# Kernel optimization log

Measured on AMD Instinct MI355X. Metric: run time of the kernel, lower is better.

Reference implementation:

```python
import jax, jax.numpy as jnp
import numpy as np

B, T, C = 1, 2048, 1024
H = 16
HD = C // H  # 64
K = 8
EPS = 1e-6
NEG = -1.0e9


def apply_rotary_emb(x, cos, sin):
    # x: (B,T,H,HD), cos/sin: (T, HD//2)
    x1, x2 = jnp.split(x, 2, axis=-1)
    c = cos[None, :, None, :]
    s = sin[None, :, None, :]
    return jnp.concatenate([x1 * c - x2 * s, x1 * s + x2 * c], axis=-1)


def rms_norm(x):
    return x * jax.lax.rsqrt(jnp.mean(jnp.square(x), axis=-1, keepdims=True) + EPS)


def setup_inputs() -> dict:
    key = jax.random.key(0)
    ks = jax.random.split(key, 8)
    x = jax.random.normal(ks[0], (B, T, C), dtype=jnp.float32)
    # standard RoPE tables
    inv_freq = 1.0 / (10000.0 ** (np.arange(0, HD, 2, dtype=np.float32) / HD))
    t = np.arange(T, dtype=np.float32)
    freqs = np.outer(t, inv_freq)  # (T, HD//2)
    cos = jnp.asarray(np.cos(freqs), dtype=jnp.float32)
    sin = jnp.asarray(np.sin(freqs), dtype=jnp.float32)
    std = 0.02
    Wq = std * jax.random.normal(ks[1], (C, C), dtype=jnp.float32)
    Wk = std * jax.random.normal(ks[2], (C, C), dtype=jnp.float32)
    Wv = std * jax.random.normal(ks[3], (C, C), dtype=jnp.float32)
    Wproj = std * jax.random.normal(ks[4], (C, C), dtype=jnp.float32)
    Wdq = jax.random.normal(ks[5], (C, K), dtype=jnp.float32) / np.sqrt(C)
    Wdk = jax.random.normal(ks[6], (C, K), dtype=jnp.float32) / np.sqrt(C)
    return {"x": x, "cos": cos, "sin": sin, "Wq": Wq, "Wk": Wk, "Wv": Wv,
            "Wproj": Wproj, "Wdq": Wdq, "Wdk": Wdk}


def reference(x, cos, sin, Wq, Wk, Wv, Wproj, Wdq, Wdk):
    b, t, c = x.shape
    q = (x @ Wq).reshape(b, t, H, HD)
    k = (x @ Wk).reshape(b, t, H, HD)
    v = (x @ Wv).reshape(b, t, H, HD)
    q = rms_norm(apply_rotary_emb(q, cos, sin))
    k = rms_norm(apply_rotary_emb(k, cos, sin))

    # digit projections (identical for every head in the source module)
    qd = x @ Wdq  # (B,T,K)
    kd = x @ Wdk  # (B,T,K)
    matches = qd[:, :, None, :] == kd[:, None, :, :]  # (B,Tq,Tk,K)
    prefix = jnp.cumprod(matches.astype(jnp.int32), axis=-1)
    lcp = jnp.sum(prefix, axis=-1)  # (B,Tq,Tk)
    lcp_mask = lcp >= (K - 1)

    causal = jnp.tril(jnp.ones((t, t), dtype=bool))
    combined = causal[None, None, :, :] & lcp_mask[:, None, :, :]  # (B,1->H,Tq,Tk)

    scale = 1.0 / jnp.sqrt(jnp.asarray(HD, x.dtype))
    scores = jnp.einsum('bqhd,bkhd->bhqk', q * scale, k)
    scores = jnp.where(combined, scores, NEG)
    w = jax.nn.softmax(scores, axis=-1)
    y = jnp.einsum('bhqk,bkhd->bqhd', w, v).reshape(b, t, c)
    return y @ Wproj
```

## Files before the change

kernel.cpp:

```cpp
#include <hip/hip_runtime.h>
#include <math.h>

#define T_DIM 2048
#define C_DIM 1024
#define H_NUM 16
#define HD_DIM 64
#define K_LCP 8
#define NEG_VAL -1.0e9f

typedef __bf16 bf16;
typedef __bf16 bf16x4 __attribute__((ext_vector_type(4)));
typedef __bf16 bf16x8 __attribute__((ext_vector_type(8)));
typedef float f32x4 __attribute__((ext_vector_type(4)));
typedef unsigned long long u64;

__global__ __launch_bounds__(256) void fused_a(
    const float* __restrict__ x, const float* __restrict__ Wdq,
    const float* __restrict__ Wdk, const float* __restrict__ Wq,
    const float* __restrict__ Wk, const float* __restrict__ Wv,
    const float* __restrict__ Wproj, bf16* __restrict__ xb,
    float* __restrict__ qd, float* __restrict__ kd, float* __restrict__ partial,
    int* __restrict__ flags, float* __restrict__ vmean,
    float* __restrict__ rowout, bf16* __restrict__ wqt, bf16* __restrict__ wkt,
    bf16* __restrict__ wvt, bf16* __restrict__ wpt) {
  __shared__ bf16 tile[64][67];
  const int vb = blockIdx.x;
  const int tid = threadIdx.x;
  if (vb < 512) {
    const int wave = tid >> 6, lane = tid & 63;
    const int t = vb * 4 + wave;
    const float* xp = x + (size_t)t * C_DIM;
    bf16* xbp = xb + (size_t)t * C_DIM;
    float aq[8] = {}, ak[8] = {};
#pragma unroll
    for (int i = 0; i < 16; ++i) {
      const int c = i * 64 + lane;
      float xv = xp[c];
      xbp[c] = (bf16)xv;
      float4 wq0 = *(const float4*)(Wdq + (size_t)c * K_LCP);
      float4 wq1 = *(const float4*)(Wdq + (size_t)c * K_LCP + 4);
      float4 wk0 = *(const float4*)(Wdk + (size_t)c * K_LCP);
      float4 wk1 = *(const float4*)(Wdk + (size_t)c * K_LCP + 4);
      aq[0] = fmaf(xv, wq0.x, aq[0]); aq[1] = fmaf(xv, wq0.y, aq[1]);
      aq[2] = fmaf(xv, wq0.z, aq[2]); aq[3] = fmaf(xv, wq0.w, aq[3]);
      aq[4] = fmaf(xv, wq1.x, aq[4]); aq[5] = fmaf(xv, wq1.y, aq[5]);
      aq[6] = fmaf(xv, wq1.z, aq[6]); aq[7] = fmaf(xv, wq1.w, aq[7]);
      ak[0] = fmaf(xv, wk0.x, ak[0]); ak[1] = fmaf(xv, wk0.y, ak[1]);
      ak[2] = fmaf(xv, wk0.z, ak[2]); ak[3] = fmaf(xv, wk0.w, ak[3]);
      ak[4] = fmaf(xv, wk1.x, ak[4]); ak[5] = fmaf(xv, wk1.y, ak[5]);
      ak[6] = fmaf(xv, wk1.z, ak[6]); ak[7] = fmaf(xv, wk1.w, ak[7]);
    }
#pragma unroll
    for (int j = 0; j < 8; ++j) {
#pragma unroll
      for (int off = 32; off >= 1; off >>= 1) {
        aq[j] += __shfl_xor(aq[j], off);
        ak[j] += __shfl_xor(ak[j], off);
      }
    }
    if (lane == 0) {
      *(float4*)(qd + (size_t)t * K_LCP) = make_float4(aq[0], aq[1], aq[2], aq[3]);
      *(float4*)(qd + (size_t)t * K_LCP + 4) = make_float4(aq[4], aq[5], aq[6], aq[7]);
      *(float4*)(kd + (size_t)t * K_LCP) = make_float4(ak[0], ak[1], ak[2], ak[3]);
      *(float4*)(kd + (size_t)t * K_LCP + 4) = make_float4(ak[4], ak[5], ak[6], ak[7]);
    }
  } else if (vb < 544) {
    const int b = vb - 512;
    if (b == 0) {
      if (tid < 112) flags[tid] = 0;
      f32x4 z = {0.f, 0.f, 0.f, 0.f};
      ((f32x4*)vmean)[tid] = z;
    }
    if (b == 1) {
      f32x4 z = {0.f, 0.f, 0.f, 0.f};
      ((f32x4*)rowout)[tid] = z;
    }
    f32x4 s = {0.f, 0.f, 0.f, 0.f};
    for (int r = 0; r < 64; ++r)
      s += ((const f32x4*)(x + (size_t)(b * 64 + r) * C_DIM))[tid];
    ((f32x4*)(partial + (size_t)b * C_DIM))[tid] = s;
  } else {
    const int idx = vb - 544;
    const int z = idx >> 8;
    const float* W = (z == 0) ? Wq : (z == 1) ? Wk : (z == 2) ? Wv : Wproj;
    bf16* O = (z == 0) ? wqt : (z == 1) ? wkt : (z == 2) ? wvt : wpt;
    const int rem = idx & 255;
    const int bk = (rem >> 4) * 64;
    const int bn = (rem & 15) * 64;
    {
      const int r = tid >> 2;
      const int c0 = (tid & 3) * 16;
      const float* src = W + (size_t)(bk + r) * C_DIM + bn + c0;
#pragma unroll
      for (int t = 0; t < 16; t += 4) {
        float4 f = *(const float4*)(src + t);
        tile[r][c0 + t + 0] = (bf16)f.x;
        tile[r][c0 + t + 1] = (bf16)f.y;
        tile[r][c0 + t + 2] = (bf16)f.z;
        tile[r][c0 + t + 3] = (bf16)f.w;
      }
    }
    __syncthreads();
    {
      const int n = tid >> 2;
      const int k0 = (tid & 3) * 16;
      bf16x8 lo, hi;
#pragma unroll
      for (int j = 0; j < 8; ++j) lo[j] = tile[k0 + j][n];
#pragma unroll
      for (int j = 0; j < 8; ++j) hi[j] = tile[k0 + 8 + j][n];
      bf16* dst = O + (size_t)(bn + n) * C_DIM + bk + k0;
      *(bf16x8*)dst = lo;
      *(bf16x8*)(dst + 8) = hi;
    }
  }
}

__global__ __launch_bounds__(256) void fused_b(
    const float* __restrict__ qd, const float* __restrict__ kd,
    const float* __restrict__ partial, const float* __restrict__ Wv,
    int* __restrict__ tilemask, int* __restrict__ allmask,
    u64* __restrict__ maskbits, float* __restrict__ vmean,
    int* __restrict__ qneed, int* __restrict__ kneed, int* __restrict__ vneed,
    int* __restrict__ pneed) {
  const int tid = threadIdx.x;
  if (blockIdx.x >= 128) {
    const int b = blockIdx.x - 128;
    const int cs = (b >> 4) * 256;
    const int jb = (b & 15) * 64;
    __shared__ float xm[256];
    __shared__ f32x4 xr[4][64];
    __shared__ float red[4][64];
    const int p = tid >> 6, t6 = tid & 63;
    {
      f32x4 s = {0.f, 0.f, 0.f, 0.f};
      for (int g = p * 8; g < p * 8 + 8; ++g)
        s += ((const f32x4*)(partial + (size_t)g * C_DIM + cs))[t6];
      xr[p][t6] = s;
      __syncthreads();
      if (p == 0) {
        f32x4 t = (xr[0][t6] + xr[1][t6]) + (xr[2][t6] + xr[3][t6]);
        t *= (1.0f / 2048.0f);
        *(f32x4*)&xm[t6 * 4] = t;
      }
      __syncthreads();
    }
    const int j = jb + t6;
    float acc = 0.f;
    for (int c = p * 64; c < p * 64 + 64; ++c)
      acc = fmaf(xm[c], Wv[(size_t)(cs + c) * C_DIM + j], acc);
    red[p][t6] = acc;
    __syncthreads();
    if (tid < 64)
      atomicAdd(&vmean[jb + tid],
                (red[0][tid] + red[1][tid]) + (red[2][tid] + red[3][tid]));
    return;
  }
  const int qb = blockIdx.x;
  __shared__ float qds[16][K_LCP];
  __shared__ int tm[32];
  const int wv = tid >> 6, lane = tid & 63;
  if (tid < 32) tm[tid] = 0;
  if (tid < 16 * K_LCP)
    qds[tid >> 3][tid & 7] = qd[(size_t)(qb * 16 + (tid >> 3)) * K_LCP + (tid & 7)];
  __syncthreads();
  const int kmax = qb * 16 + 15;
  for (int it = 0; it < 8; ++it) {
    const int kbase = it * 256 + wv * 64;
    if (kbase > kmax) break;
    const int key = kbase + lane;
    float kv[K_LCP];
    *(float4*)&kv[0] = *(const float4*)(kd + (size_t)key * K_LCP);
    *(float4*)&kv[4] = *(const float4*)(kd + (size_t)key * K_LCP + 4);
    const int grp = it * 4 + wv;
    u64 anyb = 0ull;
#pragma unroll
    for (int ql = 0; ql < 16; ++ql) {
      const int qg = qb * 16 + ql;
      bool p = (key <= qg) & (qds[ql][0] == kv[0]) & (qds[ql][1] == kv[1]) &
               (qds[ql][2] == kv[2]) & (qds[ql][3] == kv[3]) &
               (qds[ql][4] == kv[4]) & (qds[ql][5] == kv[5]) &
               (qds[ql][6] == kv[6]);
      u64 b = __ballot(p);
      anyb |= b;
      if (lane == 0) maskbits[(size_t)qg * 32 + grp] = b;
    }
    if (lane == 0 && anyb) tm[grp] = 1;
  }
  __syncthreads();
  int anytm = 0;
#pragma unroll
  for (int i = 0; i < 32; ++i) anytm |= tm[i];
  if (tid < 32) tilemask[qb * 32 + tid] = tm[tid];
  if (tid == 0) allmask[qb] = !anytm;
  if (anytm) {
    if (tid < 32) {
      if (tm[tid]) atomicOr(&kneed[tid >> 1], 1);
      atomicOr(&vneed[tid >> 1], 1);
    }
    if (tid == 0) {
      atomicOr(&qneed[qb >> 3], 1);
      atomicOr(&pneed[qb >> 2], 1);
    }
  }
}

template <int TMt, int MI, int NA>
__device__ void gemm_body(bf16* As, bf16* Bs, const bf16* A, const bf16* Bt,
                          void* Cv, int bx, int by, int z, int mode,
                          const float* cosT, const float* sinT, float* vtsum) {
  const int tid = threadIdx.x;
  const int Kd = C_DIM, N = C_DIM;
  const int bm = by * TMt;
  const int bn = bx * 128;
  const int wave = tid >> 6, lane = tid & 63;
  const int lr = lane >> 2;
  const int lc = (lane & 3) * 8;
  bf16* gA = (bf16*)(A + (size_t)(bm + wave * 16 * NA + lr) * Kd + lc);
  bf16* gB = (bf16*)(Bt + (size_t)(bn + wave * 32 + lr) * Kd + lc);
  bf16* lA = As + wave * 512 * NA;
  bf16* lB = Bs + wave * 1024;
  const int wr = (wave >> 1) * (MI * 16);
  const int wc = (wave & 1) * 64;
  const int fm = lane & 15;
  const int fk_ = (lane >> 4) * 8;

  f32x4 acc[MI][4] = {};
  for (int k0 = 0; k0 < Kd; k0 += 32) {
    __syncthreads();
#pragma unroll
    for (int u = 0; u < NA; ++u)
      __builtin_amdgcn_global_load_lds(
          (__attribute__((address_space(1))) void*)(gA + (size_t)u * 16 * Kd + k0),
          (__attribute__((address_space(3))) void*)(lA + u * 512), 16, 0, 0);
#pragma unroll
    for (int u = 0; u < 2; ++u)
      __builtin_amdgcn_global_load_lds(
          (__attribute__((address_space(1))) void*)(gB + (size_t)u * 16 * Kd + k0),
          (__attribute__((address_space(3))) void*)(lB + u * 512), 16, 0, 0);
    __syncthreads();
    bf16x8 af[MI], bfr[4];
#pragma unroll
    for (int i = 0; i < MI; ++i)
      af[i] = *(const bf16x8*)(As + (size_t)(wr + i * 16 + fm) * 32 + fk_);
#pragma unroll
    for (int j = 0; j < 4; ++j)
      bfr[j] = *(const bf16x8*)(Bs + (size_t)(wc + j * 16 + fm) * 32 + fk_);
#pragma unroll
    for (int i = 0; i < MI; ++i)
#pragma unroll
      for (int j = 0; j < 4; ++j)
        acc[i][j] = __builtin_amdgcn_mfma_f32_16x16x32_bf16(af[i], bfr[j],
                                                            acc[i][j], 0, 0, 0);
  }
  const int cq = (lane >> 4) * 4;
  if (mode && z < 2) {
    bf16* C = (bf16*)Cv;
#pragma unroll
    for (int i = 0; i < MI; ++i)
#pragma unroll
      for (int r = 0; r < 4; ++r) {
        const int t = bm + wr + i * 16 + cq + r;
        float c0 = cosT[(size_t)t * 32 + fm], s0 = sinT[(size_t)t * 32 + fm];
        float c1 = cosT[(size_t)t * 32 + 16 + fm];
        float s1 = sinT[(size_t)t * 32 + 16 + fm];
        float a0 = acc[i][0][r], a1 = acc[i][1][r];
        float a2 = acc[i][2][r], a3 = acc[i][3][r];
        float o0 = a0 * c0 - a2 * s0, o2 = a0 * s0 + a2 * c0;
        float o1 = a1 * c1 - a3 * s1, o3 = a1 * s1 + a3 * c1;
        float ss = o0 * o0 + o1 * o1 + o2 * o2 + o3 * o3;
        ss += __shfl_xor(ss, 1);
        ss += __shfl_xor(ss, 2);
        ss += __shfl_xor(ss, 4);
        ss += __shfl_xor(ss, 8);
        float rn = 1.0f / sqrtf(ss * (1.0f / 64.0f) + 1e-6f);
        size_t base = (size_t)t * N + bn + wc + fm;
        C[base + 0] = (bf16)(o0 * rn);
        C[base + 16] = (bf16)(o1 * rn);
        C[base + 32] = (bf16)(o2 * rn);
        C[base + 48] = (bf16)(o3 * rn);
      }
  } else if (mode) {
    bf16* C = (bf16*)Cv;
#pragma unroll
    for (int i = 0; i < MI; ++i)
#pragma unroll
      for (int r = 0; r < 4; ++r) {
        size_t base = (size_t)(bm + wr + i * 16 + cq + r) * N + bn + wc + fm;
#pragma unroll
        for (int j = 0; j < 4; ++j) C[base + j * 16] = (bf16)acc[i][j][r];
      }
    const int kt = (bm + wr) >> 6;
#pragma unroll
    for (int j = 0; j < 4; ++j) {
      float s = 0.f;
#pragma unroll
      for (int i = 0; i < MI; ++i)
#pragma unroll
        for (int r = 0; r < 4; ++r) s += acc[i][j][r];
      s += __shfl_xor(s, 16);
      s += __shfl_xor(s, 32);
      if ((lane >> 4) == 0)
        vtsum[(size_t)kt * C_DIM + bn + wc + j * 16 + fm] = s;
    }
  } else {
    float* C = (float*)Cv;
#pragma unroll
    for (int i = 0; i < MI; ++i)
#pragma unroll
      for (int r = 0; r < 4; ++r) {
        size_t base = (size_t)(bm + wr + i * 16 + cq + r) * N + bn + wc + fm;
#pragma unroll
        for (int j = 0; j < 4; ++j) C[base + j * 16] = acc[i][j][r];
      }
  }
}

__global__ __launch_bounds__(256) void phase_c(
    const bf16* __restrict__ xb, const bf16* __restrict__ wqt,
    const bf16* __restrict__ wkt, const bf16* __restrict__ wvt,
    bf16* __restrict__ qB, bf16* __restrict__ kB, bf16* __restrict__ vB,
    float* __restrict__ vtsum, const float* __restrict__ cosT,
    const float* __restrict__ sinT, const int* __restrict__ qneed,
    const int* __restrict__ kneed, const int* __restrict__ vneed,
    const float* __restrict__ vmean, const float* __restrict__ Wproj,
    float* __restrict__ rowout) {
  __shared__ __align__(16) bf16 As[128 * 32];
  __shared__ __align__(16) bf16 Bs[128 * 32];
  const int vb = blockIdx.x;
  const int tid = threadIdx.x;
  if (vb < 384) {
    const int z = vb >> 7, r = vb & 127, by = r >> 3, bx = r & 7;
    const int* f = (z == 0) ? qneed : (z == 1) ? kneed : vneed;
    if (!f[by]) return;
    const bf16* Bt = (z == 0) ? wqt : (z == 1) ? wkt : wvt;
    void* C = (z == 0) ? (void*)qB : (z == 1) ? (void*)kB : (void*)vB;
    gemm_body<128, 4, 2>(As, Bs, xb, Bt, C, bx, by, z, 1, cosT, sinT, vtsum);
  } else {
    __shared__ float red[4][64];
    const int b = vb - 384;
    const int cs = (b >> 4) * 256;
    const int jb = (b & 15) * 64;
    const int p = tid >> 6, t6 = tid & 63;
    const int j = jb + t6;
    float acc = 0.f;
    for (int c = cs + p * 64; c < cs + p * 64 + 64; ++c)
      acc = fmaf(vmean[c], Wproj[(size_t)c * C_DIM + j], acc);
    red[p][t6] = acc;
    __syncthreads();
    if (tid < 64)
      atomicAdd(&rowout[jb + tid],
                (red[0][tid] + red[1][tid]) + (red[2][tid] + red[3][tid]));
  }
}

__device__ inline void write_vmean16(const float* vmp, bf16* yp) {
  f32x4 a0 = ((const f32x4*)vmp)[0];
  f32x4 a1 = ((const f32x4*)vmp)[1];
  f32x4 a2 = ((const f32x4*)vmp)[2];
  f32x4 a3 = ((const f32x4*)vmp)[3];
  bf16x8 o0 = {(bf16)a0[0], (bf16)a0[1], (bf16)a0[2], (bf16)a0[3],
               (bf16)a1[0], (bf16)a1[1], (bf16)a1[2], (bf16)a1[3]};
  bf16x8 o1 = {(bf16)a2[0], (bf16)a2[1], (bf16)a2[2], (bf16)a2[3],
               (bf16)a3[0], (bf16)a3[1], (bf16)a3[2], (bf16)a3[3]};
  *(bf16x8*)yp = o0;
  *(bf16x8*)(yp + 8) = o1;
}

__global__ __launch_bounds__(256) void attn2(
    const bf16* __restrict__ q, const bf16* __restrict__ k,
    const bf16* __restrict__ v, const float* __restrict__ vtsum,
    const float* __restrict__ vmean, const u64* __restrict__ maskbits,
    const int* __restrict__ tilemask, const int* __restrict__ allmask,
    const int* __restrict__ pneed, bf16* __restrict__ y) {
  const int h = blockIdx.y;
  const int q0 = blockIdx.x * 64;
  const int tid = threadIdx.x;
  const int wv = tid >> 6;
  const int lane = tid & 63;
  const int qb0 = q0 >> 4;

  const int a0 = allmask[qb0 + 0], a1 = allmask[qb0 + 1];
  const int a2 = allmask[qb0 + 2], a3 = allmask[qb0 + 3];
  const int pn = pneed[q0 >> 6];
  if (a0 & a1 & a2 & a3) {
    if (pn) {
      const int row = tid >> 2, d0 = (tid & 3) * 16;
      write_vmean16(vmean + h * HD_DIM + d0,
                    y + (size_t)(q0 + row) * C_DIM + h * HD_DIM + d0);
    }
    return;
  }
  const int w_active = !((wv == 0) ? a0 : (wv == 1) ? a1 : (wv == 2) ? a2 : a3);

  __shared__ __align__(16) bf16 vsT[64][72];
  __shared__ __align__(16) bf16 ps[4][16][72];
  __shared__ int tmS[4][32];
  if (tid < 128)
    tmS[tid >> 5][tid & 31] = tilemask[(size_t)(qb0 + (tid >> 5)) * 32 + (tid & 31)];

  if (!w_active && pn) {
    const int row = wv * 16 + (lane >> 2), d0 = (lane & 3) * 16;
    write_vmean16(vmean + h * HD_DIM + d0,
                  y + (size_t)(q0 + row) * C_DIM + h * HD_DIM + d0);
  }

  const int fm = lane & 15;
  const int fk = (lane >> 4) * 8;
  bf16x8 aq0 = {}, aq1 = {};
  if (w_active) {
    const bf16* qp = q + (size_t)(q0 + wv * 16 + fm) * C_DIM + h * HD_DIM;
    aq0 = *(const bf16x8*)(qp + fk);
    aq1 = *(const bf16x8*)(qp + 32 + fk);
  }
  __syncthreads();

  float m[4] = {-INFINITY, -INFINITY, -INFINITY, -INFINITY};
  float l[4] = {0.f, 0.f, 0.f, 0.f};
  f32x4 out[4] = {};

  for (int kt = 0; kt < T_DIM / 64; ++kt) {
    const int need = tmS[0][kt] | tmS[1][kt] | tmS[2][kt] | tmS[3][kt];
    const int k0 = kt * 64;
    if (need) {
      __syncthreads();
      {
        const int row = tid & 63, d0 = (tid >> 6) * 16;
        const bf16* vp = v + (size_t)(k0 + row) * C_DIM + h * HD_DIM + d0;
        bf16x8 v0 = *(const bf16x8*)(vp);
        bf16x8 v1 = *(const bf16x8*)(vp + 8);
#pragma unroll
        for (int i = 0; i < 8; ++i) vsT[d0 + i][row] = v0[i];
#pragma unroll
        for (int i = 0; i < 8; ++i) vsT[d0 + 8 + i][row] = v1[i];
      }
      __syncthreads();
    }
    if (!w_active) continue;
    if (tmS[wv][kt]) {
      u64 mwr[4];
#pragma unroll
      for (int r = 0; r < 4; ++r)
        mwr[r] = maskbits[(size_t)(q0 + wv * 16 + (lane >> 4) * 4 + r) * 32 + kt] >> fm;
      f32x4 s[4] = {};
#pragma unroll
      for (int j = 0; j < 4; ++j) {
        const bf16* kp = k + (size_t)(k0 + j * 16 + fm) * C_DIM + h * HD_DIM;
        bf16x8 bk0 = *(const bf16x8*)(kp + fk);
        bf16x8 bk1 = *(const bf16x8*)(kp + 32 + fk);
        s[j] = __builtin_amdgcn_mfma_f32_16x16x32_bf16(aq0, bk0, s[j], 0, 0, 0);
        s[j] = __builtin_amdgcn_mfma_f32_16x16x32_bf16(aq1, bk1, s[j], 0, 0, 0);
      }
      float xv[4][4];
      float tmax[4] = {NEG_VAL, NEG_VAL, NEG_VAL, NEG_VAL};
#pragma unroll
      for (int j = 0; j < 4; ++j)
#pragma unroll
        for (int r = 0; r < 4; ++r) {
          float val = ((mwr[r] >> (16 * j)) & 1ull) ? s[j][r] * 0.125f : NEG_VAL;
          xv[j][r] = val;
          tmax[r] = fmaxf(tmax[r], val);
        }
#pragma unroll
      for (int r = 0; r < 4; ++r) {
#pragma unroll
        for (int off = 1; off < 16; off <<= 1)
          tmax[r] = fmaxf(tmax[r], __shfl_xor(tmax[r], off));
      }
      float alpha[4], lsum[4] = {0.f, 0.f, 0.f, 0.f};
#pragma unroll
      for (int r = 0; r < 4; ++r) {
        float mn = fmaxf(m[r], tmax[r]);
        alpha[r] = __expf(m[r] - mn);
        m[r] = mn;
      }
#pragma unroll
      for (int j = 0; j < 4; ++j)
#pragma unroll
        for (int r = 0; r < 4; ++r) {
          float p = __expf(xv[j][r] - m[r]);
          lsum[r] += p;
          ps[wv][(lane >> 4) * 4 + r][j * 16 + fm] = (bf16)p;
        }
#pragma unroll
      for (int r = 0; r < 4; ++r) {
#pragma unroll
        for (int off = 1; off < 16; off <<= 1) lsum[r] += __shfl_xor(lsum[r], off);
        l[r] = l[r] * alpha[r] + lsum[r];
      }
#pragma unroll
      for (int jd = 0; jd < 4; ++jd)
#pragma unroll
        for (int r = 0; r < 4; ++r) out[jd][r] *= alpha[r];
      bf16x8 pa0 = *(const bf16x8*)&ps[wv][fm][fk];
      bf16x8 pa1 = *(const bf16x8*)&ps[wv][fm][32 + fk];
#pragma unroll
      for (int jd = 0; jd < 4; ++jd) {
        bf16x8 bv0 = *(const bf16x8*)&vsT[jd * 16 + fm][fk];
        bf16x8 bv1 = *(const bf16x8*)&vsT[jd * 16 + fm][32 + fk];
        out[jd] = __builtin_amdgcn_mfma_f32_16x16x32_bf16(pa0, bv0, out[jd], 0, 0, 0);
        out[jd] = __builtin_amdgcn_mfma_f32_16x16x32_bf16(pa1, bv1, out[jd], 0, 0, 0);
      }
    } else {
      int needu = (m[0] <= NEG_VAL) | (m[1] <= NEG_VAL) | (m[2] <= NEG_VAL) |
                  (m[3] <= NEG_VAL);
      if (needu) {
#pragma unroll
        for (int jd = 0; jd < 4; ++jd) {
          float vt = vtsum[(size_t)kt * C_DIM + h * HD_DIM + jd * 16 + fm];
#pragma unroll
          for (int r = 0; r < 4; ++r)
            if (m[r] <= NEG_VAL) out[jd][r] += vt;
        }
#pragma unroll
        for (int r = 0; r < 4; ++r)
          if (m[r] <= NEG_VAL) {
            m[r] = NEG_VAL;
            l[r] += 64.f;
          }
      }
    }
  }

  if (w_active) {
#pragma unroll
    for (int r = 0; r < 4; ++r) {
      float inv_l = 1.0f / l[r];
      bf16* yp = y + (size_t)(q0 + wv * 16 + (lane >> 4) * 4 + r) * C_DIM +
                 h * HD_DIM + fm;
#pragma unroll
      for (int jd = 0; jd < 4; ++jd) yp[jd * 16] = (bf16)(out[jd][r] * inv_l);
    }
  }
}

__global__ __launch_bounds__(256) void phase_e(
    const bf16* __restrict__ yb, const bf16* __restrict__ wpt,
    float* __restrict__ out, const int* __restrict__ pneed,
    const float* __restrict__ rowout, const float* __restrict__ cosT,
    const float* __restrict__ sinT) {
  __shared__ __align__(16) bf16 As[64 * 32];
  __shared__ __align__(16) bf16 Bs[128 * 32];
  const int vb = blockIdx.x;
  if (vb < 256) {
    const int by = vb >> 3, bx = vb & 7;
    if (!pneed[by]) return;
    gemm_body<64, 2, 1>(As, Bs, yb, wpt, (void*)out, bx, by, 2, 0, cosT, sinT,
                        nullptr);
  } else {
    const int b = vb - 256;
    f32x4 v = ((const f32x4*)rowout)[threadIdx.x];
#pragma unroll
    for (int r = 0; r < 8; ++r) {
      const int row = b * 8 + r;
      if (pneed[row >> 6]) continue;
      ((f32x4*)(out + (size_t)row * C_DIM))[threadIdx.x] = v;
    }
  }
}

extern "C" void kernel_launch(void* const* d_in, const int* in_sizes, int n_in,
                              void* d_out, int out_size, void* d_ws, size_t ws_size,
                              hipStream_t stream) {
  const float* x = (const float*)d_in[0];
  const float* cosT = (const float*)d_in[1];
  const float* sinT = (const float*)d_in[2];
  const float* Wq = (const float*)d_in[3];
  const float* Wk = (const float*)d_in[4];
  const float* Wv = (const float*)d_in[5];
  const float* Wproj = (const float*)d_in[6];
  const float* Wdq = (const float*)d_in[7];
  const float* Wdk = (const float*)d_in[8];
  float* out = (float*)d_out;

  char* ws = (char*)d_ws;
  const size_t TC2 = (size_t)T_DIM * C_DIM * 2;
  const size_t CC2 = (size_t)C_DIM * C_DIM * 2;
  bf16* xb = (bf16*)(ws + 0);
  bf16* wqt = (bf16*)(ws + TC2);
  bf16* wkt = (bf16*)(ws + TC2 + CC2);
  bf16* wvt = (bf16*)(ws + TC2 + 2 * CC2);
  bf16* wpt = (bf16*)(ws + TC2 + 3 * CC2);
  bf16* qB = (bf16*)(ws + TC2 + 4 * CC2);
  bf16* kB = (bf16*)(ws + 2 * TC2 + 4 * CC2);
  bf16* vB = (bf16*)(ws + 3 * TC2 + 4 * CC2);
  char* p2 = ws + 4 * TC2 + 4 * CC2;
  float* qd = (float*)p2;        p2 += (size_t)T_DIM * K_LCP * 4;
  float* kd = (float*)p2;        p2 += (size_t)T_DIM * K_LCP * 4;
  float* vtsum = (float*)p2;     p2 += 32 * C_DIM * 4;
  float* vmean = (float*)p2;     p2 += C_DIM * 4;
  float* partial = (float*)p2;   p2 += 32 * C_DIM * 4;
  float* rowout = (float*)p2;    p2 += C_DIM * 4;
  int* tilemask = (int*)p2;      p2 += (T_DIM / 16) * 32 * 4;
  int* allmask = (int*)p2;       p2 += (T_DIM / 16) * 4;
  u64* maskbits = (u64*)p2;      p2 += (size_t)T_DIM * 32 * 8;
  int* qneed = (int*)p2;         p2 += 16 * 4;
  int* kneed = (int*)p2;         p2 += 16 * 4;
  int* vneed = (int*)p2;         p2 += 16 * 4;
  int* pneed = (int*)p2;         p2 += 32 * 4;
  bf16* yb = xb;

  fused_a<<<1568, 256, 0, stream>>>(x, Wdq, Wdk, Wq, Wk, Wv, Wproj, xb, qd, kd,
                                    partial, qneed, vmean, rowout, wqt, wkt,
                                    wvt, wpt);
  fused_b<<<192, 256, 0, stream>>>(qd, kd, partial, Wv, tilemask, allmask,
                                   maskbits, vmean, qneed, kneed, vneed, pneed);
  phase_c<<<448, 256, 0, stream>>>(xb, wqt, wkt, wvt, qB, kB, vB, vtsum, cosT,
                                   sinT, qneed, kneed, vneed, vmean, Wproj,
                                   rowout);
  attn2<<<dim3(T_DIM / 64, H_NUM), 256, 0, stream>>>(
      qB, kB, vB, vtsum, vmean, maskbits, tilemask, allmask, pneed, yb);
  phase_e<<<512, 256, 0, stream>>>(yb, wpt, out, pneed, rowout, cosT, sinT);
}
```

Baseline: 134.6 us.

## Merge five kernels into one persistent kernel with grid-wide barriers

Replaces the five separate launches with one persistent 256-block kernel that runs each phase in turn and separates them with atomic-counter grid barriers, zeroing control state with a memset beforehand. It also adds an early-exit path: when no query-key pair passes the mask, it skips the bf16 casts, weight transposes, QKV GEMM and attention, and writes the broadcast row output directly. The aim is to remove launch gaps and tail effects between phases. In exchange, the fixed 256-block grid gives less parallelism in the GEMM and attention phases, and the spin barriers depend on every block being resident at once.

```diff
diff --git a/kernel.cpp b/kernel.cpp
--- a/kernel.cpp
+++ b/kernel.cpp
@@ -7,6 +7,7 @@
 #define HD_DIM 64
 #define K_LCP 8
 #define NEG_VAL -1.0e9f
+#define NBLK 256
 
 typedef __bf16 bf16;
 typedef __bf16 bf16x4 __attribute__((ext_vector_type(4)));
@@ -14,195 +15,30 @@
 typedef float f32x4 __attribute__((ext_vector_type(4)));
 typedef unsigned long long u64;
 
-__global__ __launch_bounds__(256) void fused_a(
-    const float* __restrict__ x, const float* __restrict__ Wdq,
-    const float* __restrict__ Wdk, const float* __restrict__ Wq,
-    const float* __restrict__ Wk, const float* __restrict__ Wv,
-    const float* __restrict__ Wproj, bf16* __restrict__ xb,
-    float* __restrict__ qd, float* __restrict__ kd, float* __restrict__ partial,
-    int* __restrict__ flags, float* __restrict__ vmean,
-    float* __restrict__ rowout, bf16* __restrict__ wqt, bf16* __restrict__ wkt,
-    bf16* __restrict__ wvt, bf16* __restrict__ wpt) {
-  __shared__ bf16 tile[64][67];
-  const int vb = blockIdx.x;
-  const int tid = threadIdx.x;
-  if (vb < 512) {
-    const int wave = tid >> 6, lane = tid & 63;
-    const int t = vb * 4 + wave;
-    const float* xp = x + (size_t)t * C_DIM;
-    bf16* xbp = xb + (size_t)t * C_DIM;
-    float aq[8] = {}, ak[8] = {};
-#pragma unroll
-    for (int i = 0; i < 16; ++i) {
-      const int c = i * 64 + lane;
-      float xv = xp[c];
-      xbp[c] = (bf16)xv;
-      float4 wq0 = *(const float4*)(Wdq + (size_t)c * K_LCP);
-      float4 wq1 = *(const float4*)(Wdq + (size_t)c * K_LCP + 4);
-      float4 wk0 = *(const float4*)(Wdk + (size_t)c * K_LCP);
-      float4 wk1 = *(const float4*)(Wdk + (size_t)c * K_LCP + 4);
-      aq[0] = fmaf(xv, wq0.x, aq[0]); aq[1] = fmaf(xv, wq0.y, aq[1]);
-      aq[2] = fmaf(xv, wq0.z, aq[2]); aq[3] = fmaf(xv, wq0.w, aq[3]);
-      aq[4] = fmaf(xv, wq1.x, aq[4]); aq[5] = fmaf(xv, wq1.y, aq[5]);
-      aq[6] = fmaf(xv, wq1.z, aq[6]); aq[7] = fmaf(xv, wq1.w, aq[7]);
-      ak[0] = fmaf(xv, wk0.x, ak[0]); ak[1] = fmaf(xv, wk0.y, ak[1]);
-      ak[2] = fmaf(xv, wk0.z, ak[2]); ak[3] = fmaf(xv, wk0.w, ak[3]);
-      ak[4] = fmaf(xv, wk1.x, ak[4]); ak[5] = fmaf(xv, wk1.y, ak[5]);
-      ak[6] = fmaf(xv, wk1.z, ak[6]); ak[7] = fmaf(xv, wk1.w, ak[7]);
-    }
-#pragma unroll
-    for (int j = 0; j < 8; ++j) {
-#pragma unroll
-      for (int off = 32; off >= 1; off >>= 1) {
-        aq[j] += __shfl_xor(aq[j], off);
-        ak[j] += __shfl_xor(ak[j], off);
-      }
-    }
-    if (lane == 0) {
-      *(float4*)(qd + (size_t)t * K_LCP) = make_float4(aq[0], aq[1], aq[2], aq[3]);
-      *(float4*)(qd + (size_t)t * K_LCP + 4) = make_float4(aq[4], aq[5], aq[6], aq[7]);
-      *(float4*)(kd + (size_t)t * K_LCP) = make_float4(ak[0], ak[1], ak[2], ak[3]);
-      *(float4*)(kd + (size_t)t * K_LCP + 4) = make_float4(ak[4], ak[5], ak[6], ak[7]);
-    }
-  } else if (vb < 544) {
-    const int b = vb - 512;
-    if (b == 0) {
-      if (tid < 112) flags[tid] = 0;
-      f32x4 z = {0.f, 0.f, 0.f, 0.f};
-      ((f32x4*)vmean)[tid] = z;
-    }
-    if (b == 1) {
-      f32x4 z = {0.f, 0.f, 0.f, 0.f};
-      ((f32x4*)rowout)[tid] = z;
-    }
-    f32x4 s = {0.f, 0.f, 0.f, 0.f};
-    for (int r = 0; r < 64; ++r)
-      s += ((const f32x4*)(x + (size_t)(b * 64 + r) * C_DIM))[tid];
-    ((f32x4*)(partial + (size_t)b * C_DIM))[tid] = s;
-  } else {
-    const int idx = vb - 544;
-    const int z = idx >> 8;
-    const float* W = (z == 0) ? Wq : (z == 1) ? Wk : (z == 2) ? Wv : Wproj;
-    bf16* O = (z == 0) ? wqt : (z == 1) ? wkt : (z == 2) ? wvt : wpt;
-    const int rem = idx & 255;
-    const int bk = (rem >> 4) * 64;
-    const int bn = (rem & 15) * 64;
-    {
-      const int r = tid >> 2;
-      const int c0 = (tid & 3) * 16;
-      const float* src = W + (size_t)(bk + r) * C_DIM + bn + c0;
-#pragma unroll
-      for (int t = 0; t < 16; t += 4) {
-        float4 f = *(const float4*)(src + t);
-        tile[r][c0 + t + 0] = (bf16)f.x;
-        tile[r][c0 + t + 1] = (bf16)f.y;
-        tile[r][c0 + t + 2] = (bf16)f.z;
-        tile[r][c0 + t + 3] = (bf16)f.w;
-      }
-    }
-    __syncthreads();
-    {
-      const int n = tid >> 2;
-      const int k0 = (tid & 3) * 16;
-      bf16x8 lo, hi;
-#pragma unroll
-      for (int j = 0; j < 8; ++j) lo[j] = tile[k0 + j][n];
-#pragma unroll
-      for (int j = 0; j < 8; ++j) hi[j] = tile[k0 + 8 + j][n];
-      bf16* dst = O + (size_t)(bn + n) * C_DIM + bk + k0;
-      *(bf16x8*)dst = lo;
-      *(bf16x8*)(dst + 8) = hi;
-    }
-  }
-}
-
-__global__ __launch_bounds__(256) void fused_b(
-    const float* __restrict__ qd, const float* __restrict__ kd,
-    const float* __restrict__ partial, const float* __restrict__ Wv,
-    int* __restrict__ tilemask, int* __restrict__ allmask,
-    u64* __restrict__ maskbits, float* __restrict__ vmean,
-    int* __restrict__ qneed, int* __restrict__ kneed, int* __restrict__ vneed,
-    int* __restrict__ pneed) {
-  const int tid = threadIdx.x;
-  if (blockIdx.x >= 128) {
-    const int b = blockIdx.x - 128;
-    const int cs = (b >> 4) * 256;
-    const int jb = (b & 15) * 64;
-    __shared__ float xm[256];
-    __shared__ f32x4 xr[4][64];
-    __shared__ float red[4][64];
-    const int p = tid >> 6, t6 = tid & 63;
-    {
-      f32x4 s = {0.f, 0.f, 0.f, 0.f};
-      for (int g = p * 8; g < p * 8 + 8; ++g)
-        s += ((const f32x4*)(partial + (size_t)g * C_DIM + cs))[t6];
-      xr[p][t6] = s;
-      __syncthreads();
-      if (p == 0) {
-        f32x4 t = (xr[0][t6] + xr[1][t6]) + (xr[2][t6] + xr[3][t6]);
-        t *= (1.0f / 2048.0f);
-        *(f32x4*)&xm[t6 * 4] = t;
-      }
-      __syncthreads();
-    }
-    const int j = jb + t6;
-    float acc = 0.f;
-    for (int c = p * 64; c < p * 64 + 64; ++c)
-      acc = fmaf(xm[c], Wv[(size_t)(cs + c) * C_DIM + j], acc);
-    red[p][t6] = acc;
-    __syncthreads();
-    if (tid < 64)
-      atomicAdd(&vmean[jb + tid],
-                (red[0][tid] + red[1][tid]) + (red[2][tid] + red[3][tid]));
-    return;
-  }
-  const int qb = blockIdx.x;
-  __shared__ float qds[16][K_LCP];
-  __shared__ int tm[32];
-  const int wv = tid >> 6, lane = tid & 63;
-  if (tid < 32) tm[tid] = 0;
-  if (tid < 16 * K_LCP)
-    qds[tid >> 3][tid & 7] = qd[(size_t)(qb * 16 + (tid >> 3)) * K_LCP + (tid & 7)];
+struct Prm {
+  const float *x, *cosT, *sinT, *Wq, *Wk, *Wv, *Wproj, *Wdq, *Wdk;
+  float* out;
+  bf16 *xb, *wqt, *wkt, *wvt, *wpt, *qB, *kB, *vB;
+  float *qd, *kd, *vtsum, *partial;
+  int *tilemask, *allmask;
+  u64* maskbits;
+  float *vmean, *rowout;
+  int* flags;
+  int* bars;
+};
+
+__device__ __forceinline__ void gbar(int* bars, int slot) {
   __syncthreads();
-  const int kmax = qb * 16 + 15;
-  for (int it = 0; it < 8; ++it) {
-    const int kbase = it * 256 + wv * 64;
-    if (kbase > kmax) break;
-    const int key = kbase + lane;
-    float kv[K_LCP];
-    *(float4*)&kv[0] = *(const float4*)(kd + (size_t)key * K_LCP);
-    *(float4*)&kv[4] = *(const float4*)(kd + (size_t)key * K_LCP + 4);
-    const int grp = it * 4 + wv;
-    u64 anyb = 0ull;
-#pragma unroll
-    for (int ql = 0; ql < 16; ++ql) {
-      const int qg = qb * 16 + ql;
-      bool p = (key <= qg) & (qds[ql][0] == kv[0]) & (qds[ql][1] == kv[1]) &
-               (qds[ql][2] == kv[2]) & (qds[ql][3] == kv[3]) &
-               (qds[ql][4] == kv[4]) & (qds[ql][5] == kv[5]) &
-               (qds[ql][6] == kv[6]);
-      u64 b = __ballot(p);
-      anyb |= b;
-      if (lane == 0) maskbits[(size_t)qg * 32 + grp] = b;
-    }
-    if (lane == 0 && anyb) tm[grp] = 1;
+  if (threadIdx.x == 0) {
+    __threadfence();
+    __hip_atomic_fetch_add(&bars[slot], 1, __ATOMIC_ACQ_REL,
+                           __HIP_MEMORY_SCOPE_AGENT);
+    while (__hip_atomic_load(&bars[slot], __ATOMIC_ACQUIRE,
+                             __HIP_MEMORY_SCOPE_AGENT) < NBLK)
+      __builtin_amdgcn_s_sleep(2);
+    __threadfence();
   }
   __syncthreads();
-  int anytm = 0;
-#pragma unroll
-  for (int i = 0; i < 32; ++i) anytm |= tm[i];
-  if (tid < 32) tilemask[qb * 32 + tid] = tm[tid];
-  if (tid == 0) allmask[qb] = !anytm;
-  if (anytm) {
-    if (tid < 32) {
-      if (tm[tid]) atomicOr(&kneed[tid >> 1], 1);
-      atomicOr(&vneed[tid >> 1], 1);
-    }
-    if (tid == 0) {
-      atomicOr(&qneed[qb >> 3], 1);
-      atomicOr(&pneed[qb >> 2], 1);
-    }
-  }
 }
 
 template <int TMt, int MI, int NA>
@@ -316,44 +152,6 @@
   }
 }
 
-__global__ __launch_bounds__(256) void phase_c(
-    const bf16* __restrict__ xb, const bf16* __restrict__ wqt,
-    const bf16* __restrict__ wkt, const bf16* __restrict__ wvt,
-    bf16* __restrict__ qB, bf16* __restrict__ kB, bf16* __restrict__ vB,
-    float* __restrict__ vtsum, const float* __restrict__ cosT,
-    const float* __restrict__ sinT, const int* __restrict__ qneed,
-    const int* __restrict__ kneed, const int* __restrict__ vneed,
-    const float* __restrict__ vmean, const float* __restrict__ Wproj,
-    float* __restrict__ rowout) {
-  __shared__ __align__(16) bf16 As[128 * 32];
-  __shared__ __align__(16) bf16 Bs[128 * 32];
-  const int vb = blockIdx.x;
-  const int tid = threadIdx.x;
-  if (vb < 384) {
-    const int z = vb >> 7, r = vb & 127, by = r >> 3, bx = r & 7;
-    const int* f = (z == 0) ? qneed : (z == 1) ? kneed : vneed;
-    if (!f[by]) return;
-    const bf16* Bt = (z == 0) ? wqt : (z == 1) ? wkt : wvt;
-    void* C = (z == 0) ? (void*)qB : (z == 1) ? (void*)kB : (void*)vB;
-    gemm_body<128, 4, 2>(As, Bs, xb, Bt, C, bx, by, z, 1, cosT, sinT, vtsum);
-  } else {
-    __shared__ float red[4][64];
-    const int b = vb - 384;
-    const int cs = (b >> 4) * 256;
-    const int jb = (b & 15) * 64;
-    const int p = tid >> 6, t6 = tid & 63;
-    const int j = jb + t6;
-    float acc = 0.f;
-    for (int c = cs + p * 64; c < cs + p * 64 + 64; ++c)
-      acc = fmaf(vmean[c], Wproj[(size_t)c * C_DIM + j], acc);
-    red[p][t6] = acc;
-    __syncthreads();
-    if (tid < 64)
-      atomicAdd(&rowout[jb + tid],
-                (red[0][tid] + red[1][tid]) + (red[2][tid] + red[3][tid]));
-  }
-}
-
 __device__ inline void write_vmean16(const float* vmp, bf16* yp) {
   f32x4 a0 = ((const f32x4*)vmp)[0];
   f32x4 a1 = ((const f32x4*)vmp)[1];
@@ -367,14 +165,15 @@
   *(bf16x8*)(yp + 8) = o1;
 }
 
-__global__ __launch_bounds__(256) void attn2(
-    const bf16* __restrict__ q, const bf16* __restrict__ k,
-    const bf16* __restrict__ v, const float* __restrict__ vtsum,
-    const float* __restrict__ vmean, const u64* __restrict__ maskbits,
-    const int* __restrict__ tilemask, const int* __restrict__ allmask,
-    const int* __restrict__ pneed, bf16* __restrict__ y) {
-  const int h = blockIdx.y;
-  const int q0 = blockIdx.x * 64;
+__device__ void attn_body(int q64, int h, const bf16* q, const bf16* k,
+                          const bf16* v, const float* vtsum,
+                          const float* vmean, const u64* maskbits,
+                          const int* tilemask, const int* allmask,
+                          const int* pneed, bf16* y, char* smem) {
+  bf16 (*vsT)[72] = (bf16(*)[72])smem;
+  bf16 (*ps)[16][72] = (bf16(*)[16][72])(smem + 9216);
+  int (*tmS)[32] = (int(*)[32])(smem + 18432);
+  const int q0 = q64 * 64;
   const int tid = threadIdx.x;
   const int wv = tid >> 6;
   const int lane = tid & 63;
@@ -393,9 +192,6 @@
   }
   const int w_active = !((wv == 0) ? a0 : (wv == 1) ? a1 : (wv == 2) ? a2 : a3);
 
-  __shared__ __align__(16) bf16 vsT[64][72];
-  __shared__ __align__(16) bf16 ps[4][16][72];
-  __shared__ int tmS[4][32];
   if (tid < 128)
     tmS[tid >> 5][tid & 31] = tilemask[(size_t)(qb0 + (tid >> 5)) * 32 + (tid & 31)];
 
@@ -478,9 +274,9 @@
       for (int j = 0; j < 4; ++j)
 #pragma unroll
         for (int r = 0; r < 4; ++r) {
-          float p = __expf(xv[j][r] - m[r]);
-          lsum[r] += p;
-          ps[wv][(lane >> 4) * 4 + r][j * 16 + fm] = (bf16)p;
+          float pp = __expf(xv[j][r] - m[r]);
+          lsum[r] += pp;
+          ps[wv][(lane >> 4) * 4 + r][j * 16 + fm] = (bf16)pp;
         }
 #pragma unroll
       for (int r = 0; r < 4; ++r) {
@@ -534,27 +330,269 @@
   }
 }
 
-__global__ __launch_bounds__(256) void phase_e(
-    const bf16* __restrict__ yb, const bf16* __restrict__ wpt,
-    float* __restrict__ out, const int* __restrict__ pneed,
-    const float* __restrict__ rowout, const float* __restrict__ cosT,
-    const float* __restrict__ sinT) {
-  __shared__ __align__(16) bf16 As[64 * 32];
-  __shared__ __align__(16) bf16 Bs[128 * 32];
-  const int vb = blockIdx.x;
-  if (vb < 256) {
-    const int by = vb >> 3, bx = vb & 7;
-    if (!pneed[by]) return;
-    gemm_body<64, 2, 1>(As, Bs, yb, wpt, (void*)out, bx, by, 2, 0, cosT, sinT,
-                        nullptr);
-  } else {
-    const int b = vb - 256;
-    f32x4 v = ((const f32x4*)rowout)[threadIdx.x];
+__global__ __launch_bounds__(256, 2) void mono(Prm p) {
+  const int gid = blockIdx.x;
+  const int tid = threadIdx.x;
+  const int wave = tid >> 6, lane = tid & 63;
+  __shared__ __align__(16) char smem[19456];
+
+  int* qneed = p.flags;
+  int* kneed = p.flags + 16;
+  int* vneed = p.flags + 32;
+  int* pneed = p.flags + 48;
+  int* anyfl = p.flags + 80;
+
+  for (int rr = 0; rr < 2; ++rr) {
+    const int t = gid * 8 + rr * 4 + wave;
+    const float* xp = p.x + (size_t)t * C_DIM;
+    float aq[8] = {}, ak[8] = {};
+#pragma unroll
+    for (int i = 0; i < 16; ++i) {
+      const int c = i * 64 + lane;
+      float xv = xp[c];
+      float4 wq0 = *(const float4*)(p.Wdq + (size_t)c * K_LCP);
+      float4 wq1 = *(const float4*)(p.Wdq + (size_t)c * K_LCP + 4);
+      float4 wk0 = *(const float4*)(p.Wdk + (size_t)c * K_LCP);
+      float4 wk1 = *(const float4*)(p.Wdk + (size_t)c * K_LCP + 4);
+      aq[0] = fmaf(xv, wq0.x, aq[0]); aq[1] = fmaf(xv, wq0.y, aq[1]);
+      aq[2] = fmaf(xv, wq0.z, aq[2]); aq[3] = fmaf(xv, wq0.w, aq[3]);
+      aq[4] = fmaf(xv, wq1.x, aq[4]); aq[5] = fmaf(xv, wq1.y, aq[5]);
+      aq[6] = fmaf(xv, wq1.z, aq[6]); aq[7] = fmaf(xv, wq1.w, aq[7]);
+      ak[0] = fmaf(xv, wk0.x, ak[0]); ak[1] = fmaf(xv, wk0.y, ak[1]);
+      ak[2] = fmaf(xv, wk0.z, ak[2]); ak[3] = fmaf(xv, wk0.w, ak[3]);
+      ak[4] = fmaf(xv, wk1.x, ak[4]); ak[5] = fmaf(xv, wk1.y, ak[5]);
+      ak[6] = fmaf(xv, wk1.z, ak[6]); ak[7] = fmaf(xv, wk1.w, ak[7]);
+    }
+#pragma unroll
+    for (int j = 0; j < 8; ++j) {
+#pragma unroll
+      for (int off = 32; off >= 1; off >>= 1) {
+        aq[j] += __shfl_xor(aq[j], off);
+        ak[j] += __shfl_xor(ak[j], off);
+      }
+    }
+    if (lane == 0) {
+      *(float4*)(p.qd + (size_t)t * K_LCP) = make_float4(aq[0], aq[1], aq[2], aq[3]);
+      *(float4*)(p.qd + (size_t)t * K_LCP + 4) = make_float4(aq[4], aq[5], aq[6], aq[7]);
+      *(float4*)(p.kd + (size_t)t * K_LCP) = make_float4(ak[0], ak[1], ak[2], ak[3]);
+      *(float4*)(p.kd + (size_t)t * K_LCP + 4) = make_float4(ak[4], ak[5], ak[6], ak[7]);
+    }
+  }
+  if (gid < 32) {
+    f32x4 s = {0.f, 0.f, 0.f, 0.f};
+    for (int r = 0; r < 64; ++r)
+      s += ((const f32x4*)(p.x + (size_t)(gid * 64 + r) * C_DIM))[tid];
+    ((f32x4*)(p.partial + (size_t)gid * C_DIM))[tid] = s;
+  }
+  gbar(p.bars, 0);
+
+  if (gid < 128) {
+    const int qb = gid;
+    float (*qds)[K_LCP] = (float(*)[K_LCP])smem;
+    int* tm = (int*)(smem + 512);
+    if (tid < 32) tm[tid] = 0;
+    if (tid < 16 * K_LCP)
+      qds[tid >> 3][tid & 7] =
+          p.qd[(size_t)(qb * 16 + (tid >> 3)) * K_LCP + (tid & 7)];
+    __syncthreads();
+    const int kmax = qb * 16 + 15;
+    for (int it = 0; it < 8; ++it) {
+      const int kbase = it * 256 + wave * 64;
+      if (kbase > kmax) break;
+      const int key = kbase + lane;
+      float kv[K_LCP];
+      *(float4*)&kv[0] = *(const float4*)(p.kd + (size_t)key * K_LCP);
+      *(float4*)&kv[4] = *(const float4*)(p.kd + (size_t)key * K_LCP + 4);
+      const int grp = it * 4 + wave;
+      u64 anyb = 0ull;
+#pragma unroll
+      for (int ql = 0; ql < 16; ++ql) {
+        const int qg = qb * 16 + ql;
+        bool pr = (key <= qg) & (qds[ql][0] == kv[0]) & (qds[ql][1] == kv[1]) &
+                  (qds[ql][2] == kv[2]) & (qds[ql][3] == kv[3]) &
+                  (qds[ql][4] == kv[4]) & (qds[ql][5] == kv[5]) &
+                  (qds[ql][6] == kv[6]);
+        u64 b = __ballot(pr);
+        anyb |= b;
+        if (lane == 0) p.maskbits[(size_t)qg * 32 + grp] = b;
+      }
+      if (lane == 0 && anyb) tm[grp] = 1;
+    }
+    __syncthreads();
+    int anytm = 0;
+#pragma unroll
+    for (int i = 0; i < 32; ++i) anytm |= tm[i];
+    if (tid < 32) p.tilemask[qb * 32 + tid] = tm[tid];
+    if (tid == 0) p.allmask[qb] = !anytm;
+    if (anytm) {
+      if (tid < 32) {
+        if (tm[tid]) atomicOr(&kneed[tid >> 1], 1);
+        atomicOr(&vneed[tid >> 1], 1);
+      }
+      if (tid == 0) {
+        atomicOr(&qneed[qb >> 3], 1);
+        atomicOr(&pneed[qb >> 2], 1);
+        atomicOr(anyfl, 1);
+      }
+    }
+  } else if (gid < 192) {
+    const int b = gid - 128;
+    const int cs = (b >> 4) * 256;
+    const int jb = (b & 15) * 64;
+    float* xm = (float*)smem;
+    f32x4 (*xr)[64] = (f32x4(*)[64])(smem + 1024);
+    float (*red)[64] = (float(*)[64])(smem + 5120);
+    const int pq = tid >> 6, t6 = tid & 63;
+    {
+      f32x4 s = {0.f, 0.f, 0.f, 0.f};
+      for (int g = pq * 8; g < pq * 8 + 8; ++g)
+        s += ((const f32x4*)(p.partial + (size_t)g * C_DIM + cs))[t6];
+      xr[pq][t6] = s;
+      __syncthreads();
+      if (pq == 0) {
+        f32x4 t = (xr[0][t6] + xr[1][t6]) + (xr[2][t6] + xr[3][t6]);
+        t *= (1.0f / 2048.0f);
+        *(f32x4*)&xm[t6 * 4] = t;
+      }
+      __syncthreads();
+    }
+    const int j = jb + t6;
+    float acc = 0.f;
+    for (int c = pq * 64; c < pq * 64 + 64; ++c)
+      acc = fmaf(xm[c], p.Wv[(size_t)(cs + c) * C_DIM + j], acc);
+    red[pq][t6] = acc;
+    __syncthreads();
+    if (tid < 64)
+      atomicAdd(&p.vmean[jb + tid],
+                (red[0][tid] + red[1][tid]) + (red[2][tid] + red[3][tid]));
+  }
+  gbar(p.bars, 1);
+
+  const int any = *anyfl;
+
+  if (!any) {
+    if (gid < 64) {
+      float (*red)[64] = (float(*)[64])smem;
+      const int cs = (gid >> 4) * 256;
+      const int jb = (gid & 15) * 64;
+      const int pq = tid >> 6, t6 = tid & 63;
+      const int j = jb + t6;
+      float acc = 0.f;
+      for (int c = cs + pq * 64; c < cs + pq * 64 + 64; ++c)
+        acc = fmaf(p.vmean[c], p.Wproj[(size_t)c * C_DIM + j], acc);
+      red[pq][t6] = acc;
+      __syncthreads();
+      if (tid < 64)
+        atomicAdd(&p.rowout[jb + tid],
+                  (red[0][tid] + red[1][tid]) + (red[2][tid] + red[3][tid]));
+    }
+    gbar(p.bars, 2);
+    f32x4 v4 = ((const f32x4*)p.rowout)[tid];
+#pragma unroll
+    for (int r = 0; r < 8; ++r)
+      ((f32x4*)(p.out + (size_t)(gid * 8 + r) * C_DIM))[tid] = v4;
+    return;
+  }
+
+  for (int rr = 0; rr < 8; ++rr) {
+    const int t = gid * 8 + rr;
+    float4 f = *(const float4*)(p.x + (size_t)t * C_DIM + tid * 4);
+    bf16x4 o = {(bf16)f.x, (bf16)f.y, (bf16)f.z, (bf16)f.w};
+    *(bf16x4*)(p.xb + (size_t)t * C_DIM + tid * 4) = o;
+  }
+  {
+    bf16 (*tile)[67] = (bf16(*)[67])smem;
+    for (int it = 0; it < 4; ++it) {
+      const int idx = gid * 4 + it;
+      const int z = idx >> 8;
+      const float* W = (z == 0) ? p.Wq : (z == 1) ? p.Wk : (z == 2) ? p.Wv : p.Wproj;
+      bf16* O = (z == 0) ? p.wqt : (z == 1) ? p.wkt : (z == 2) ? p.wvt : p.wpt;
+      const int rem = idx & 255;
+      const int bk = (rem >> 4) * 64;
+      const int bn = (rem & 15) * 64;
+      __syncthreads();
+      {
+        const int r = tid >> 2;
+        const int c0 = (tid & 3) * 16;
+        const float* src = W + (size_t)(bk + r) * C_DIM + bn + c0;
+#pragma unroll
+        for (int t = 0; t < 16; t += 4) {
+          float4 f = *(const float4*)(src + t);
+          tile[r][c0 + t + 0] = (bf16)f.x;
+          tile[r][c0 + t + 1] = (bf16)f.y;
+          tile[r][c0 + t + 2] = (bf16)f.z;
+          tile[r][c0 + t + 3] = (bf16)f.w;
+        }
+      }
+      __syncthreads();
+      {
+        const int n = tid >> 2;
+        const int k0 = (tid & 3) * 16;
+        bf16x8 lo, hi;
+#pragma unroll
+        for (int j = 0; j < 8; ++j) lo[j] = tile[k0 + j][n];
+#pragma unroll
+        for (int j = 0; j < 8; ++j) hi[j] = tile[k0 + 8 + j][n];
+        bf16* dst = O + (size_t)(bn + n) * C_DIM + bk + k0;
+        *(bf16x8*)dst = lo;
+        *(bf16x8*)(dst + 8) = hi;
+      }
+    }
+  }
+  if (gid < 64) {
+    __syncthreads();
+    float (*red)[64] = (float(*)[64])smem;
+    const int cs = (gid >> 4) * 256;
+    const int jb = (gid & 15) * 64;
+    const int pq = tid >> 6, t6 = tid & 63;
+    const int j = jb + t6;
+    float acc = 0.f;
+    for (int c = cs + pq * 64; c < cs + pq * 64 + 64; ++c)
+      acc = fmaf(p.vmean[c], p.Wproj[(size_t)c * C_DIM + j], acc);
+    red[pq][t6] = acc;
+    __syncthreads();
+    if (tid < 64)
+      atomicAdd(&p.rowout[jb + tid],
+                (red[0][tid] + red[1][tid]) + (red[2][tid] + red[3][tid]));
+  }
+  gbar(p.bars, 2);
+
+  {
+    bf16* As = (bf16*)smem;
+    bf16* Bs = (bf16*)(smem + 8192);
+    for (int v = gid; v < 384; v += 256) {
+      __syncthreads();
+      const int z = v >> 7, r = v & 127, by = r >> 3, bx = r & 7;
+      const int* f = (z == 0) ? qneed : (z == 1) ? kneed : vneed;
+      if (!f[by]) continue;
+      const bf16* Bt = (z == 0) ? p.wqt : (z == 1) ? p.wkt : p.wvt;
+      void* C = (z == 0) ? (void*)p.qB : (z == 1) ? (void*)p.kB : (void*)p.vB;
+      gemm_body<128, 4, 2>(As, Bs, p.xb, Bt, C, bx, by, z, 1, p.cosT, p.sinT,
+                           p.vtsum);
+    }
+  }
+  gbar(p.bars, 3);
+
+  for (int v = gid; v < 512; v += 256) {
+    __syncthreads();
+    attn_body(v & 31, v >> 5, p.qB, p.kB, p.vB, p.vtsum, p.vmean, p.maskbits,
+              p.tilemask, p.allmask, pneed, p.xb , smem);
+  }
+  gbar(p.bars, 4);
+
+  {
+    bf16* As = (bf16*)smem;
+    bf16* Bs = (bf16*)(smem + 8192);
+    const int by = gid >> 3, bx = gid & 7;
+    if (pneed[by])
+      gemm_body<64, 2, 1>(As, Bs, p.xb , p.wpt, (void*)p.out, bx, by, 2,
+                          0, p.cosT, p.sinT, nullptr);
+    f32x4 v4 = ((const f32x4*)p.rowout)[tid];
 #pragma unroll
     for (int r = 0; r < 8; ++r) {
-      const int row = b * 8 + r;
-      if (pneed[row >> 6]) continue;
-      ((f32x4*)(out + (size_t)row * C_DIM))[threadIdx.x] = v;
+      const int row = gid * 8 + r;
+      if (!pneed[row >> 6])
+        ((f32x4*)(p.out + (size_t)row * C_DIM))[tid] = v4;
     }
   }
 }
@@ -562,53 +600,43 @@
 extern "C" void kernel_launch(void* const* d_in, const int* in_sizes, int n_in,
                               void* d_out, int out_size, void* d_ws, size_t ws_size,
                               hipStream_t stream) {
-  const float* x = (const float*)d_in[0];
-  const float* cosT = (const float*)d_in[1];
-  const float* sinT = (const float*)d_in[2];
-  const float* Wq = (const float*)d_in[3];
-  const float* Wk = (const float*)d_in[4];
-  const float* Wv = (const float*)d_in[5];
-  const float* Wproj = (const float*)d_in[6];
-  const float* Wdq = (const float*)d_in[7];
-  const float* Wdk = (const float*)d_in[8];
-  float* out = (float*)d_out;
-
   char* ws = (char*)d_ws;
   const size_t TC2 = (size_t)T_DIM * C_DIM * 2;
   const size_t CC2 = (size_t)C_DIM * C_DIM * 2;
-  bf16* xb = (bf16*)(ws + 0);
-  bf16* wqt = (bf16*)(ws + TC2);
-  bf16* wkt = (bf16*)(ws + TC2 + CC2);
-  bf16* wvt = (bf16*)(ws + TC2 + 2 * CC2);
-  bf16* wpt = (bf16*)(ws + TC2 + 3 * CC2);
-  bf16* qB = (bf16*)(ws + TC2 + 4 * CC2);
-  bf16* kB = (bf16*)(ws + 2 * TC2 + 4 * CC2);
-  bf16* vB = (bf16*)(ws + 3 * TC2 + 4 * CC2);
+  Prm p;
+  p.x = (const float*)d_in[0];
+  p.cosT = (const float*)d_in[1];
+  p.sinT = (const float*)d_in[2];
+  p.Wq = (const float*)d_in[3];
+  p.Wk = (const float*)d_in[4];
+  p.Wv = (const float*)d_in[5];
+  p.Wproj = (const float*)d_in[6];
+  p.Wdq = (const float*)d_in[7];
+  p.Wdk = (const float*)d_in[8];
+  p.out = (float*)d_out;
+  p.xb = (bf16*)(ws + 0);
+  p.wqt = (bf16*)(ws + TC2);
+  p.wkt = (bf16*)(ws + TC2 + CC2);
+  p.wvt = (bf16*)(ws + TC2 + 2 * CC2);
+  p.wpt = (bf16*)(ws + TC2 + 3 * CC2);
+  p.qB = (bf16*)(ws + TC2 + 4 * CC2);
+  p.kB = (bf16*)(ws + 2 * TC2 + 4 * CC2);
+  p.vB = (bf16*)(ws + 3 * TC2 + 4 * CC2);
   char* p2 = ws + 4 * TC2 + 4 * CC2;
-  float* qd = (float*)p2;        p2 += (size_t)T_DIM * K_LCP * 4;
-  float* kd = (float*)p2;        p2 += (size_t)T_DIM * K_LCP * 4;
-  float* vtsum = (float*)p2;     p2 += 32 * C_DIM * 4;
-  float* vmean = (float*)p2;     p2 += C_DIM * 4;
-  float* partial = (float*)p2;   p2 += 32 * C_DIM * 4;
-  float* rowout = (float*)p2;    p2 += C_DIM * 4;
-  int* tilemask = (int*)p2;      p2 += (T_DIM / 16) * 32 * 4;
-  int* allmask = (int*)p2;       p2 += (T_DIM / 16) * 4;
-  u64* maskbits = (u64*)p2;      p2 += (size_t)T_DIM * 32 * 8;
-  int* qneed = (int*)p2;         p2 += 16 * 4;
-  int* kneed = (int*)p2;         p2 += 16 * 4;
-  int* vneed = (int*)p2;         p2 += 16 * 4;
-  int* pneed = (int*)p2;         p2 += 32 * 4;
-  bf16* yb = xb;
-
-  fused_a<<<1568, 256, 0, stream>>>(x, Wdq, Wdk, Wq, Wk, Wv, Wproj, xb, qd, kd,
-                                    partial, qneed, vmean, rowout, wqt, wkt,
-                                    wvt, wpt);
-  fused_b<<<192, 256, 0, stream>>>(qd, kd, partial, Wv, tilemask, allmask,
-                                   maskbits, vmean, qneed, kneed, vneed, pneed);
-  phase_c<<<448, 256, 0, stream>>>(xb, wqt, wkt, wvt, qB, kB, vB, vtsum, cosT,
-                                   sinT, qneed, kneed, vneed, vmean, Wproj,
-                                   rowout);
-  attn2<<<dim3(T_DIM / 64, H_NUM), 256, 0, stream>>>(
-      qB, kB, vB, vtsum, vmean, maskbits, tilemask, allmask, pneed, yb);
-  phase_e<<<512, 256, 0, stream>>>(yb, wpt, out, pneed, rowout, cosT, sinT);
+  p.qd = (float*)p2;      p2 += (size_t)T_DIM * K_LCP * 4;
+  p.kd = (float*)p2;      p2 += (size_t)T_DIM * K_LCP * 4;
+  p.vtsum = (float*)p2;   p2 += 32 * C_DIM * 4;
+  p.partial = (float*)p2; p2 += 32 * C_DIM * 4;
+  p.tilemask = (int*)p2;  p2 += (T_DIM / 16) * 32 * 4;
+  p.allmask = (int*)p2;   p2 += (T_DIM / 16) * 4;
+  p.maskbits = (u64*)p2;  p2 += (size_t)T_DIM * 32 * 8;
+  char* ctrl = p2;
+  p.vmean = (float*)p2;   p2 += C_DIM * 4;
+  p.rowout = (float*)p2;  p2 += C_DIM * 4;
+  p.flags = (int*)p2;     p2 += 128 * 4;
+  p.bars = (int*)p2;      p2 += 16 * 4;
+  const size_t ctrl_bytes = (size_t)(p2 - ctrl);
+
+  hipMemsetAsync(ctrl, 0, ctrl_bytes, stream);
+  mono<<<NBLK, 256, 0, stream>>>(p);
 }
```

After: 262.4 us. 95.0% more time.
